# Performance work log

Hardware: AMD Instinct MI355X
Metric: run time of the kernel (lower is better)

The kernel has to match this reference:

```python
import jax, jax.numpy as jnp
import numpy as np

SR = 3                       # search_range
NSIDE = 2 * SR + 1
N2 = NSIDE * NSIDE           # 49 block-match candidates


def _spiral_order(sz):
    """Indices of the (2sz+1)^2 flattened grid in center-out spiral order."""
    n = 2 * sz + 1
    i = j = 0
    order = [(j + sz) * n + (i + sz)]
    dirs = [(1, 0), (0, 1), (-1, 0), (0, -1)]  # right, down, left, up
    d, step = 0, 1
    while len(order) < n * n:
        for _ in range(2):
            di, dj = dirs[d]
            for _ in range(step):
                i += di; j += dj
                if abs(i) <= sz and abs(j) <= sz:
                    order.append((j + sz) * n + (i + sz))
            d = (d + 1) % 4
        step += 1
    return np.asarray(order, dtype=np.int32)


def _vec_lut(sz):
    rng = np.arange(-sz, sz + 1)
    jj, ii = np.meshgrid(rng, rng, indexing='ij')
    return (-1.0 * np.stack([jj, ii], axis=-1).reshape(-1, 2)).astype(np.float16)


SPIRAL = jnp.asarray(_spiral_order(SR))   # [49]
VEC_LUT = jnp.asarray(_vec_lut(SR))       # [49, 2] fp16


def setup_inputs() -> dict:
    key = jax.random.key(0)
    k1, k2 = jax.random.split(key)
    shape = (1, 270, 480, N2 + 1, 16)  # [B,H,W,N=50,K2=16]; last candidate = input MV
    w1 = jax.random.randint(k1, shape, 0, 256).astype(jnp.float16)
    w2 = jax.random.randint(k2, shape, 0, 256).astype(jnp.float16)
    return {"w1": w1, "w2": w2}


def reference(w1, w2):
    B, H, W, Ncand, K2 = w1.shape
    # abs-diff cost volume (int16 SAD, accumulated in int32)
    diff = jnp.abs(w1.astype(jnp.int16) - w2.astype(jnp.int16))
    cost = jnp.sum(diff, axis=-1, dtype=jnp.int32)          # [B,H,W,Ncand]

    # spiral-centered argmin over the 49 block-match candidates:
    # permute into center-out spiral order, take first-occurrence argmin
    # (tie-break toward center), map back to original flat index.
    cost_bm = cost[..., :N2]
    k = jnp.argmin(cost_bm[..., SPIRAL], axis=-1)           # [B,H,W]
    min_idx_bm = SPIRAL[k]                                   # [B,H,W]
    min_cost_bm = jnp.take_along_axis(cost, min_idx_bm[..., None], axis=3)  # [B,H,W,1]

    has_input_mv = (Ncand - 1 == N2)  # static shape check
    if has_input_mv:
        cost_at_input_mv = cost[..., -1:]
        input_mv_mask = cost_at_input_mv < min_cost_bm
        min_idx = jnp.where(input_mv_mask, N2, min_idx_bm[..., None])
        min_cost_volume = jnp.minimum(cost_at_input_mv, min_cost_bm)
    else:
        input_mv_mask = jnp.zeros_like(min_cost_bm, dtype=bool)
        min_idx = min_idx_bm[..., None]
        min_cost_volume = min_cost_bm

    vector = VEC_LUT[min_idx_bm]                             # [B,H,W,2] fp16 (block-match only)
    idx = jnp.broadcast_to(min_idx[..., None], (B, H, W, 1, K2)).astype(jnp.int32)
    min_templates = jnp.take_along_axis(w1, idx, axis=3)     # [B,H,W,1,K2]
    return (vector, min_templates, input_mv_mask, min_cost_volume)
```

## Files before the change

### kernel.cpp

```cpp
#include <hip/hip_runtime.h>
#include <stdint.h>

#define NPIX     129600
#define NC       50
#define N2       49
#define OUT_TMPL 259200
#define OUT_MASK 2332800
#define OUT_COST 2462400

__constant__ unsigned char RANKLUT[49] = {
  42,43,44,45,46,47,48,
  41,20,21,22,23,24,25,
  40,19, 6, 7, 8, 9,26,
  39,18, 5, 0, 1,10,27,
  38,17, 4, 3, 2,11,28,
  37,16,15,14,13,12,29,
  36,35,34,33,32,31,30
};

__global__ __launch_bounds__(256) void cv_kernel(
    const float* __restrict__ w1,
    const float* __restrict__ w2,
    float* __restrict__ out)
{
  const int wave = threadIdx.x >> 6;
  const int lane = threadIdx.x & 63;
  const int p = blockIdx.x * 4 + wave;

  float A[16];
#pragma unroll
  for (int r = 0; r < 16; ++r) A[r] = 0.f;
  int cost = 0;
  if (lane < NC) {
    const float4* pa = (const float4*)(w1 + (size_t)p * (NC * 16) + lane * 16);
    const float4* pb = (const float4*)(w2 + (size_t)p * (NC * 16) + lane * 16);
    float4 a0 = pa[0], a1 = pa[1], a2 = pa[2], a3 = pa[3];
    float4 b0 = pb[0], b1 = pb[1], b2 = pb[2], b3 = pb[3];
    A[0]=a0.x; A[1]=a0.y; A[2]=a0.z; A[3]=a0.w;
    A[4]=a1.x; A[5]=a1.y; A[6]=a1.z; A[7]=a1.w;
    A[8]=a2.x; A[9]=a2.y; A[10]=a2.z; A[11]=a2.w;
    A[12]=a3.x; A[13]=a3.y; A[14]=a3.z; A[15]=a3.w;
    float B[16] = {b0.x,b0.y,b0.z,b0.w, b1.x,b1.y,b1.z,b1.w,
                   b2.x,b2.y,b2.z,b2.w, b3.x,b3.y,b3.z,b3.w};
    float s = 0.f;
#pragma unroll
    for (int r = 0; r < 16; ++r) s += fabsf(A[r] - B[r]);
    cost = (int)s;
  }

  int key = (lane < N2) ? ((cost << 12) | ((int)RANKLUT[lane] << 6) | lane)
                        : 0x7FFFFFFF;
#pragma unroll
  for (int m = 32; m >= 1; m >>= 1) {
    int o = __shfl_xor(key, m, 64);
    key = min(key, o);
  }
  const int cost49   = __shfl(cost, N2, 64);
  const int flat_bm  = key & 63;
  const int cost_bm  = key >> 12;
  const bool mv      = cost49 < cost_bm;
  const int min_cost = mv ? cost49 : cost_bm;
  const int min_idx  = mv ? N2 : flat_bm;

  float t[16];
#pragma unroll
  for (int r = 0; r < 16; ++r) t[r] = __shfl(A[r], min_idx, 64);

  if (lane == 0) {
    float4* tp = (float4*)(out + OUT_TMPL + (size_t)p * 16);
    tp[0] = make_float4(t[0],  t[1],  t[2],  t[3]);
    tp[1] = make_float4(t[4],  t[5],  t[6],  t[7]);
    tp[2] = make_float4(t[8],  t[9],  t[10], t[11]);
    tp[3] = make_float4(t[12], t[13], t[14], t[15]);
    const int jj = flat_bm / 7 - 3;
    const int ii = flat_bm % 7 - 3;
    *(float2*)(out + (size_t)p * 2) = make_float2((float)(-jj), (float)(-ii));
    out[OUT_MASK + p] = mv ? 1.0f : 0.0f;
    out[OUT_COST + p] = (float)min_cost;
  }
}

extern "C" void kernel_launch(void* const* d_in, const int* in_sizes, int n_in,
                              void* d_out, int out_size, void* d_ws, size_t ws_size,
                              hipStream_t stream) {
  const float* w1 = (const float*)d_in[0];
  const float* w2 = (const float*)d_in[1];
  float* out = (float*)d_out;
  dim3 grid(NPIX / 4);
  dim3 block(256);
  cv_kernel<<<grid, block, 0, stream>>>(w1, w2, out);
}
```

Measured before the change: 153.6 us.

## Stream costs through LDS with fully coalesced float4 loads per 32-pixel block

Each block now handles 32 pixels. All 256 threads read contiguous float4s of w1 and w2, reduce groups of four lanes into per-candidate SADs, and stage those costs as u16 in shared memory. Each wave then runs the spiral argmin for 8 pixels from LDS and re-fetches the winning template row from global memory instead of shuffling 16 registers. This gives perfectly coalesced streaming loads with no idle lanes, in exchange for a barrier, a small re-read of w1, and u16 cost truncation, which holds because the maximum SAD is 16*255.

```diff
diff --git a/kernel.cpp b/kernel.cpp
--- a/kernel.cpp
+++ b/kernel.cpp
@@ -1,9 +1,13 @@
 #include <hip/hip_runtime.h>
 #include <stdint.h>
+
+typedef unsigned short u16;
 
 #define NPIX     129600
 #define NC       50
 #define N2       49
+#define PXB      32
+#define NITER    25
 #define OUT_TMPL 259200
 #define OUT_MASK 2332800
 #define OUT_COST 2462400
@@ -23,60 +27,60 @@
     const float* __restrict__ w2,
     float* __restrict__ out)
 {
-  const int wave = threadIdx.x >> 6;
-  const int lane = threadIdx.x & 63;
-  const int p = blockIdx.x * 4 + wave;
+  __shared__ u16 lds_cost[PXB * NC];
 
-  float A[16];
+  const int tid  = threadIdx.x;
+  const int lane = tid & 63;
+  const int wv   = tid >> 6;
+  const int P0   = blockIdx.x * PXB;
+  const long B4  = (long)P0 * 200;
+
+  const float4* w1v = (const float4*)w1;
+  const float4* w2v = (const float4*)w2;
+
+#pragma unroll 5
+  for (int i = 0; i < NITER; ++i) {
+    const int F = i * 256 + tid;
+    float4 a = w1v[B4 + F];
+    float4 b = w2v[B4 + F];
+    float s = fabsf(a.x - b.x) + fabsf(a.y - b.y)
+            + fabsf(a.z - b.z) + fabsf(a.w - b.w);
+    s += __shfl_xor(s, 1, 64);
+    s += __shfl_xor(s, 2, 64);
+    if ((tid & 3) == 0) lds_cost[i * 64 + (tid >> 2)] = (u16)(int)s;
+  }
+  __syncthreads();
+
+  for (int k = 0; k < PXB / 4; ++k) {
+    const int lp = wv * 8 + k;
+    const int p  = P0 + lp;
+
+    const int cost = (lane < NC) ? (int)lds_cost[lp * NC + lane] : 0x7FFFF;
+    int key = (lane < N2) ? ((cost << 12) | ((int)RANKLUT[lane] << 6) | lane)
+                          : 0x7FFFFFFF;
 #pragma unroll
-  for (int r = 0; r < 16; ++r) A[r] = 0.f;
-  int cost = 0;
-  if (lane < NC) {
-    const float4* pa = (const float4*)(w1 + (size_t)p * (NC * 16) + lane * 16);
-    const float4* pb = (const float4*)(w2 + (size_t)p * (NC * 16) + lane * 16);
-    float4 a0 = pa[0], a1 = pa[1], a2 = pa[2], a3 = pa[3];
-    float4 b0 = pb[0], b1 = pb[1], b2 = pb[2], b3 = pb[3];
-    A[0]=a0.x; A[1]=a0.y; A[2]=a0.z; A[3]=a0.w;
-    A[4]=a1.x; A[5]=a1.y; A[6]=a1.z; A[7]=a1.w;
-    A[8]=a2.x; A[9]=a2.y; A[10]=a2.z; A[11]=a2.w;
-    A[12]=a3.x; A[13]=a3.y; A[14]=a3.z; A[15]=a3.w;
-    float B[16] = {b0.x,b0.y,b0.z,b0.w, b1.x,b1.y,b1.z,b1.w,
-                   b2.x,b2.y,b2.z,b2.w, b3.x,b3.y,b3.z,b3.w};
-    float s = 0.f;
-#pragma unroll
-    for (int r = 0; r < 16; ++r) s += fabsf(A[r] - B[r]);
-    cost = (int)s;
-  }
+    for (int m = 32; m >= 1; m >>= 1) {
+      int o = __shfl_xor(key, m, 64);
+      key = min(key, o);
+    }
+    const int cost49   = (int)lds_cost[lp * NC + N2];
+    const int flat_bm  = key & 63;
+    const int cost_bm  = key >> 12;
+    const bool mv      = cost49 < cost_bm;
+    const int min_cost = mv ? cost49 : cost_bm;
+    const int min_idx  = mv ? N2 : flat_bm;
 
-  int key = (lane < N2) ? ((cost << 12) | ((int)RANKLUT[lane] << 6) | lane)
-                        : 0x7FFFFFFF;
-#pragma unroll
-  for (int m = 32; m >= 1; m >>= 1) {
-    int o = __shfl_xor(key, m, 64);
-    key = min(key, o);
-  }
-  const int cost49   = __shfl(cost, N2, 64);
-  const int flat_bm  = key & 63;
-  const int cost_bm  = key >> 12;
-  const bool mv      = cost49 < cost_bm;
-  const int min_cost = mv ? cost49 : cost_bm;
-  const int min_idx  = mv ? N2 : flat_bm;
-
-  float t[16];
-#pragma unroll
-  for (int r = 0; r < 16; ++r) t[r] = __shfl(A[r], min_idx, 64);
-
-  if (lane == 0) {
-    float4* tp = (float4*)(out + OUT_TMPL + (size_t)p * 16);
-    tp[0] = make_float4(t[0],  t[1],  t[2],  t[3]);
-    tp[1] = make_float4(t[4],  t[5],  t[6],  t[7]);
-    tp[2] = make_float4(t[8],  t[9],  t[10], t[11]);
-    tp[3] = make_float4(t[12], t[13], t[14], t[15]);
-    const int jj = flat_bm / 7 - 3;
-    const int ii = flat_bm % 7 - 3;
-    *(float2*)(out + (size_t)p * 2) = make_float2((float)(-jj), (float)(-ii));
-    out[OUT_MASK + p] = mv ? 1.0f : 0.0f;
-    out[OUT_COST + p] = (float)min_cost;
+    if (lane < 4) {
+      float4 t = w1v[(long)p * 200 + min_idx * 4 + lane];
+      ((float4*)out)[OUT_TMPL / 4 + p * 4 + lane] = t;
+    }
+    if (lane == 0) {
+      const int jj = flat_bm / 7 - 3;
+      const int ii = flat_bm % 7 - 3;
+      *(float2*)(out + (long)p * 2) = make_float2((float)(-jj), (float)(-ii));
+      out[OUT_MASK + p] = mv ? 1.0f : 0.0f;
+      out[OUT_COST + p] = (float)min_cost;
+    }
   }
 }
 
@@ -86,7 +90,7 @@
   const float* w1 = (const float*)d_in[0];
   const float* w2 = (const float*)d_in[1];
   float* out = (float*)d_out;
-  dim3 grid(NPIX / 4);
+  dim3 grid(NPIX / PXB);
   dim3 block(256);
   cv_kernel<<<grid, block, 0, stream>>>(w1, w2, out);
 }
```

Result: slower. 164.8 us (+7.3%).
